# Kernel optimization log

Hardware: AMD Instinct MI355X
Metric: run time of the kernel (lower is better)

Reference implementation:

```python
import jax, jax.numpy as jnp
import numpy as np

HIDDEN = 160
LN_EPS = 1e-5


def _gru_dir(x_seq, Wih, Whh, bih, bhh, reverse):
    # x_seq: [B,T,D] -> hidden states [B,T,H] (PyTorch GRU gate math)
    B = x_seq.shape[0]
    xW = jnp.einsum('btd,gd->btg', x_seq, Wih) + bih  # [B,T,3H]
    if reverse:
        xW = xW[:, ::-1]

    def step(h, xw):
        g = h @ Whh.T + bhh
        xr, xz, xn = jnp.split(xw, 3, axis=-1)
        hr, hz, hn = jnp.split(g, 3, axis=-1)
        r = jax.nn.sigmoid(xr + hr)
        z = jax.nn.sigmoid(xz + hz)
        n = jnp.tanh(xn + r * hn)
        h_new = (1.0 - z) * n + z * h
        return h_new, h_new

    h0 = jnp.zeros((B, HIDDEN), dtype=x_seq.dtype)
    _, hs = jax.lax.scan(step, h0, jnp.swapaxes(xW, 0, 1))  # [T,B,H]
    hs = jnp.swapaxes(hs, 0, 1)  # [B,T,H]
    if reverse:
        hs = hs[:, ::-1]
    return hs


def _bigru_layer(x_seq, Wih, Whh, bih, bhh):
    f = _gru_dir(x_seq, Wih[0], Whh[0], bih[0], bhh[0], False)
    b = _gru_dir(x_seq, Wih[1], Whh[1], bih[1], bhh[1], True)
    return jnp.concatenate([f, b], axis=-1)  # [B,T,2H]


def setup_inputs() -> dict:
    key = jax.random.key(0)
    ks = jax.random.split(key, 16)
    s = 0.1  # keep activations in a sane range
    d = {
        'x': jax.random.normal(ks[0], (64, 512, 128), jnp.float32),
        'Wih0': s * jax.random.normal(ks[1], (2, 480, 128), jnp.float32),
        'Whh0': s * jax.random.normal(ks[2], (2, 480, 160), jnp.float32),
        'bih0': s * jax.random.normal(ks[3], (2, 480), jnp.float32),
        'bhh0': s * jax.random.normal(ks[4], (2, 480), jnp.float32),
        'Wih1': s * jax.random.normal(ks[5], (2, 480, 320), jnp.float32),
        'Whh1': s * jax.random.normal(ks[6], (2, 480, 160), jnp.float32),
        'bih1': s * jax.random.normal(ks[7], (2, 480), jnp.float32),
        'bhh1': s * jax.random.normal(ks[8], (2, 480), jnp.float32),
        'key_w': s * jax.random.normal(ks[9], (160, 320), jnp.float32),
        'key_b': s * jax.random.normal(ks[10], (160,), jnp.float32),
        'score_w': s * jax.random.normal(ks[11], (4, 160), jnp.float32),
        'score_b': s * jax.random.normal(ks[12], (4,), jnp.float32),
        'proj_w': s * jax.random.normal(ks[13], (256, 320), jnp.float32),
        'proj_b': s * jax.random.normal(ks[14], (256,), jnp.float32),
        'ln_g': jnp.ones((256,), jnp.float32),
        'ln_b': jnp.zeros((256,), jnp.float32),
    }
    return d


def reference(x, Wih0, Whh0, bih0, bhh0, Wih1, Whh1, bih1, bhh1,
              key_w, key_b, score_w, score_b, proj_w, proj_b, ln_g, ln_b):
    # bi-GRU, 2 layers (dropout off in eval)
    h1 = _bigru_layer(x, Wih0, Whh0, bih0, bhh0)   # [B,T,2H]
    seq_out = _bigru_layer(h1, Wih1, Whh1, bih1, bhh1)  # [B,T,2H]

    keys = jnp.tanh(seq_out @ key_w.T + key_b)           # [B,T,H]
    attn_logits = keys @ score_w.T + score_b             # [B,T,heads]

    # motion bias: per-frame displacement norm, z-normalized over time (std is unbiased)
    motion = jnp.linalg.norm(x[:, 1:] - x[:, :-1], axis=-1, keepdims=True)  # [B,T-1,1]
    motion = jnp.concatenate([motion[:, :1], motion], axis=1)               # [B,T,1]
    motion = (motion - motion.mean(axis=1, keepdims=True)) / (
        motion.std(axis=1, keepdims=True, ddof=1) + 1e-6)

    weights = jax.nn.softmax(attn_logits + motion, axis=1)  # [B,T,heads]

    # sum over time of per-head weighted seq_out, then mean over heads
    n_heads = weights.shape[-1]
    pooled = jnp.einsum('btd,bth->bd', seq_out, weights) / n_heads  # [B,2H]

    embedding = pooled @ proj_w.T + proj_b  # dropout=identity in eval
    mu = embedding.mean(axis=-1, keepdims=True)
    var = embedding.var(axis=-1, keepdims=True)
    embedding = (embedding - mu) * jax.lax.rsqrt(var + LN_EPS) * ln_g + ln_b
    embedding = embedding / jnp.maximum(
        jnp.linalg.norm(embedding, axis=-1, keepdims=True), 1e-12)

    return embedding, weights.mean(axis=2)
```

## Files before the change

kernel.cpp:

```cpp
#include <hip/hip_runtime.h>
#include <hip/hip_bf16.h>
#include <math.h>

#define T_SEQ 512
#define BATCH 64
#define DIN   128
#define H     160
#define G3    480

typedef _Float16 half8_t __attribute__((ext_vector_type(8)));
typedef _Float16 half4_t __attribute__((ext_vector_type(4)));
typedef _Float16 half2_t __attribute__((ext_vector_type(2)));
typedef float    f32x4   __attribute__((ext_vector_type(4)));

__device__ __forceinline__ float sigmoidf_(float x) {
    return 1.0f / (1.0f + __expf(-x));
}
__device__ __forceinline__ float tanhf_(float x) {
    float a = fabsf(x);
    float e = __expf(2.0f * a);
    float t = 1.0f - 2.0f / (e + 1.0f);
    return copysignf(t, x);
}

__device__ __forceinline__ void dot8(const half8_t h, const half8_t w,
                                     float& a0, float& a1, float& a2, float& a3) {
#if __has_builtin(__builtin_amdgcn_fdot2)
    half2_t h01{h[0], h[1]}, h23{h[2], h[3]}, h45{h[4], h[5]}, h67{h[6], h[7]};
    half2_t w01{w[0], w[1]}, w23{w[2], w[3]}, w45{w[4], w[5]}, w67{w[6], w[7]};
    a0 = __builtin_amdgcn_fdot2(h01, w01, a0, false);
    a1 = __builtin_amdgcn_fdot2(h23, w23, a1, false);
    a2 = __builtin_amdgcn_fdot2(h45, w45, a2, false);
    a3 = __builtin_amdgcn_fdot2(h67, w67, a3, false);
#else
    a0 += (float)h[0] * (float)w[0] + (float)h[1] * (float)w[1];
    a1 += (float)h[2] * (float)w[2] + (float)h[3] * (float)w[3];
    a2 += (float)h[4] * (float)w[4] + (float)h[5] * (float)w[5];
    a3 += (float)h[6] * (float)w[6] + (float)h[7] * (float)w[7];
#endif
}

__device__ __forceinline__ float blockReduceSum(float v, float* red) {
    #pragma unroll
    for (int off = 32; off > 0; off >>= 1) v += __shfl_down(v, off, 64);
    int wave = threadIdx.x >> 6, lane = threadIdx.x & 63;
    __syncthreads();
    if (lane == 0) red[wave] = v;
    __syncthreads();
    float s = red[0];
    int nw = blockDim.x >> 6;
    for (int i = 1; i < nw; ++i) s += red[i];
    return s;
}
__device__ __forceinline__ float blockReduceMax(float v, float* red) {
    #pragma unroll
    for (int off = 32; off > 0; off >>= 1) v = fmaxf(v, __shfl_down(v, off, 64));
    int wave = threadIdx.x >> 6, lane = threadIdx.x & 63;
    __syncthreads();
    if (lane == 0) red[wave] = v;
    __syncthreads();
    float s = red[0];
    int nw = blockDim.x >> 6;
    for (int i = 1; i < nw; ++i) s = fmaxf(s, red[i]);
    return s;
}

__global__ __launch_bounds__(256) void cvt_f2h_kernel(
    const float* __restrict__ src, _Float16* __restrict__ dst, int n4)
{
    int i = blockIdx.x * 256 + threadIdx.x;
    int stride = gridDim.x * 256;
    for (; i < n4; i += stride) {
        float4 v = reinterpret_cast<const float4*>(src)[i];
        half4_t h = {(_Float16)v.x, (_Float16)v.y, (_Float16)v.z, (_Float16)v.w};
        reinterpret_cast<half4_t*>(dst)[i] = h;
    }
}

template<int LDSK>
__global__ __launch_bounds__(256) void gemm_f16_mfma_kernel(
    const _Float16* __restrict__ A, const _Float16* __restrict__ B,
    const float* __restrict__ bias, float* __restrict__ C,
    int N, int K, int act)
{
    __shared__ _Float16 Bs[64][LDSK];
    int tid  = threadIdx.x;
    int lane = tid & 63, wave = tid >> 6;
    int row0 = blockIdx.x * 64, col0 = blockIdx.y * 64;
    int kc8 = K >> 3;
    for (int idx = tid; idx < 64 * kc8; idx += 256) {
        int rr = idx / kc8, kc = (idx - rr * kc8) << 3;
        int gcol = col0 + rr;
        half8_t v = {};
        if (gcol < N) v = *reinterpret_cast<const half8_t*>(B + (size_t)gcol * K + kc);
        *reinterpret_cast<half8_t*>(&Bs[rr][kc]) = v;
    }
    __syncthreads();

    f32x4 acc0 = {}, acc1 = {}, acc2 = {}, acc3 = {};
    int arow = row0 + wave * 16 + (lane & 15);
    int koff = (lane >> 4) << 3;
    const _Float16* ap = A + (size_t)arow * K + koff;
    int bl = lane & 15;
    for (int k0 = 0; k0 < K; k0 += 32) {
        half8_t a8 = *reinterpret_cast<const half8_t*>(ap + k0);
        half8_t b0 = *reinterpret_cast<const half8_t*>(&Bs[bl     ][k0 + koff]);
        half8_t b1 = *reinterpret_cast<const half8_t*>(&Bs[bl + 16][k0 + koff]);
        half8_t b2 = *reinterpret_cast<const half8_t*>(&Bs[bl + 32][k0 + koff]);
        half8_t b3 = *reinterpret_cast<const half8_t*>(&Bs[bl + 48][k0 + koff]);
        acc0 = __builtin_amdgcn_mfma_f32_16x16x32_f16(a8, b0, acc0, 0, 0, 0);
        acc1 = __builtin_amdgcn_mfma_f32_16x16x32_f16(a8, b1, acc1, 0, 0, 0);
        acc2 = __builtin_amdgcn_mfma_f32_16x16x32_f16(a8, b2, acc2, 0, 0, 0);
        acc3 = __builtin_amdgcn_mfma_f32_16x16x32_f16(a8, b3, acc3, 0, 0, 0);
    }

    int crow = row0 + wave * 16 + ((lane >> 4) << 2);
    int cb   = col0 + (lane & 15);
    f32x4 accs[4] = {acc0, acc1, acc2, acc3};
    #pragma unroll
    for (int j = 0; j < 4; ++j) {
        int ccol = cb + j * 16;
        if (ccol < N) {
            float bv = bias[ccol];
            #pragma unroll
            for (int i = 0; i < 4; ++i) {
                float v = accs[j][i] + bv;
                if (act) v = tanhf_(v);
                C[(size_t)(crow + i) * N + ccol] = v;
            }
        }
    }
}

__global__ __launch_bounds__(512)
__attribute__((amdgpu_waves_per_eu(2, 2)))
void gru_kernel(
    const float* __restrict__ xw, const _Float16* __restrict__ whh_h,
    const float* __restrict__ bhh, _Float16* __restrict__ out)
{
    int b    = blockIdx.x >> 1;
    int dir  = blockIdx.x & 1;
    int tid  = threadIdx.x;
    bool active = (tid < G3);
    int rc   = active ? tid : 0;
    __shared__ __align__(16) _Float16 h_h[H];
    __shared__ float g_s[G3];

    const _Float16* wp = whh_h + (size_t)dir * G3 * H + (size_t)rc * H;
    float4 f0, f1, f2, f3, f4, f5, f6, f7, f8, f9;
    float4 f10, f11, f12, f13, f14, f15, f16, f17, f18, f19;
    asm volatile("global_load_dwordx4 %0, %1, off"            : "=&v"(f0)  : "v"(wp));
    asm volatile("global_load_dwordx4 %0, %1, off offset:16"  : "=&v"(f1)  : "v"(wp));
    asm volatile("global_load_dwordx4 %0, %1, off offset:32"  : "=&v"(f2)  : "v"(wp));
    asm volatile("global_load_dwordx4 %0, %1, off offset:48"  : "=&v"(f3)  : "v"(wp));
    asm volatile("global_load_dwordx4 %0, %1, off offset:64"  : "=&v"(f4)  : "v"(wp));
    asm volatile("global_load_dwordx4 %0, %1, off offset:80"  : "=&v"(f5)  : "v"(wp));
    asm volatile("global_load_dwordx4 %0, %1, off offset:96"  : "=&v"(f6)  : "v"(wp));
    asm volatile("global_load_dwordx4 %0, %1, off offset:112" : "=&v"(f7)  : "v"(wp));
    asm volatile("global_load_dwordx4 %0, %1, off offset:128" : "=&v"(f8)  : "v"(wp));
    asm volatile("global_load_dwordx4 %0, %1, off offset:144" : "=&v"(f9)  : "v"(wp));
    asm volatile("global_load_dwordx4 %0, %1, off offset:160" : "=&v"(f10) : "v"(wp));
    asm volatile("global_load_dwordx4 %0, %1, off offset:176" : "=&v"(f11) : "v"(wp));
    asm volatile("global_load_dwordx4 %0, %1, off offset:192" : "=&v"(f12) : "v"(wp));
    asm volatile("global_load_dwordx4 %0, %1, off offset:208" : "=&v"(f13) : "v"(wp));
    asm volatile("global_load_dwordx4 %0, %1, off offset:224" : "=&v"(f14) : "v"(wp));
    asm volatile("global_load_dwordx4 %0, %1, off offset:240" : "=&v"(f15) : "v"(wp));
    asm volatile("global_load_dwordx4 %0, %1, off offset:256" : "=&v"(f16) : "v"(wp));
    asm volatile("global_load_dwordx4 %0, %1, off offset:272" : "=&v"(f17) : "v"(wp));
    asm volatile("global_load_dwordx4 %0, %1, off offset:288" : "=&v"(f18) : "v"(wp));
    asm volatile("global_load_dwordx4 %0, %1, off offset:304" : "=&v"(f19) : "v"(wp));
    float bias = bhh[dir * G3 + rc];
    asm volatile("s_waitcnt vmcnt(0)" ::: "memory");
    __builtin_amdgcn_sched_barrier(0);
    half8_t w0  = __builtin_bit_cast(half8_t, f0);
    half8_t w1  = __builtin_bit_cast(half8_t, f1);
    half8_t w2  = __builtin_bit_cast(half8_t, f2);
    half8_t w3  = __builtin_bit_cast(half8_t, f3);
    half8_t w4  = __builtin_bit_cast(half8_t, f4);
    half8_t w5  = __builtin_bit_cast(half8_t, f5);
    half8_t w6  = __builtin_bit_cast(half8_t, f6);
    half8_t w7  = __builtin_bit_cast(half8_t, f7);
    half8_t w8  = __builtin_bit_cast(half8_t, f8);
    half8_t w9  = __builtin_bit_cast(half8_t, f9);
    half8_t w10 = __builtin_bit_cast(half8_t, f10);
    half8_t w11 = __builtin_bit_cast(half8_t, f11);
    half8_t w12 = __builtin_bit_cast(half8_t, f12);
    half8_t w13 = __builtin_bit_cast(half8_t, f13);
    half8_t w14 = __builtin_bit_cast(half8_t, f14);
    half8_t w15 = __builtin_bit_cast(half8_t, f15);
    half8_t w16 = __builtin_bit_cast(half8_t, f16);
    half8_t w17 = __builtin_bit_cast(half8_t, f17);
    half8_t w18 = __builtin_bit_cast(half8_t, f18);
    half8_t w19 = __builtin_bit_cast(half8_t, f19);

    if (tid < H) h_h[tid] = (_Float16)0.f;
    float hcur = 0.f;
    __syncthreads();

    float xr = 0.f, xz = 0.f, xn = 0.f;
    {
        int tt0 = dir ? (T_SEQ - 1) : 0;
        size_t base0 = ((size_t)b * T_SEQ + tt0) * 960 + (size_t)dir * G3;
        if (tid < H) {
            xr = xw[base0 + tid];
            xz = xw[base0 + H + tid];
            xn = xw[base0 + 2 * H + tid];
        }
    }

    for (int step = 0; step < T_SEQ; ++step) {
        int tt = dir ? (T_SEQ - 1 - step) : step;
        float nxr = 0.f, nxz = 0.f, nxn = 0.f;
        {
            int sn  = (step + 1 < T_SEQ) ? step + 1 : step;
            int ttn = dir ? (T_SEQ - 1 - sn) : sn;
            size_t basen = ((size_t)b * T_SEQ + ttn) * 960 + (size_t)dir * G3;
            if (tid < H) {
                nxr = xw[basen + tid];
                nxz = xw[basen + H + tid];
                nxn = xw[basen + 2 * H + tid];
            }
        }
        float a0 = 0.f, a1 = 0.f, a2 = 0.f, a3 = 0.f;
        {
            const half8_t* hp8 = reinterpret_cast<const half8_t*>(h_h);
            dot8(hp8[0],  w0,  a0, a1, a2, a3);
            dot8(hp8[1],  w1,  a0, a1, a2, a3);
            dot8(hp8[2],  w2,  a0, a1, a2, a3);
            dot8(hp8[3],  w3,  a0, a1, a2, a3);
            dot8(hp8[4],  w4,  a0, a1, a2, a3);
            dot8(hp8[5],  w5,  a0, a1, a2, a3);
            dot8(hp8[6],  w6,  a0, a1, a2, a3);
            dot8(hp8[7],  w7,  a0, a1, a2, a3);
            dot8(hp8[8],  w8,  a0, a1, a2, a3);
            dot8(hp8[9],  w9,  a0, a1, a2, a3);
            dot8(hp8[10], w10, a0, a1, a2, a3);
            dot8(hp8[11], w11, a0, a1, a2, a3);
            dot8(hp8[12], w12, a0, a1, a2, a3);
            dot8(hp8[13], w13, a0, a1, a2, a3);
            dot8(hp8[14], w14, a0, a1, a2, a3);
            dot8(hp8[15], w15, a0, a1, a2, a3);
            dot8(hp8[16], w16, a0, a1, a2, a3);
            dot8(hp8[17], w17, a0, a1, a2, a3);
            dot8(hp8[18], w18, a0, a1, a2, a3);
            dot8(hp8[19], w19, a0, a1, a2, a3);
        }
        if (active) g_s[tid] = (a0 + a1) + (a2 + a3) + bias;
        __syncthreads();
        if (tid < H) {
            float rg = sigmoidf_(xr + g_s[tid]);
            float z  = sigmoidf_(xz + g_s[H + tid]);
            float n  = tanhf_(xn + rg * g_s[2 * H + tid]);
            float hn = (1.0f - z) * n + z * hcur;
            hcur = hn;
            h_h[tid] = (_Float16)hn;
            out[((size_t)b * T_SEQ + tt) * 320 + (size_t)dir * H + tid] = (_Float16)hn;
        }
        __syncthreads();
        xr = nxr; xz = nxz; xn = nxn;
    }
}

__global__ __launch_bounds__(256) void logits_kernel(
    const float* __restrict__ keys, const float* __restrict__ sw,
    const float* __restrict__ sb, float* __restrict__ out)
{
    int gid = blockIdx.x * 256 + threadIdx.x;
    int tok = gid >> 2, h = gid & 3;
    const float4* kr = reinterpret_cast<const float4*>(keys + (size_t)tok * H);
    const float4* wr = reinterpret_cast<const float4*>(sw + (size_t)h * H);
    float acc = 0.f;
    #pragma unroll
    for (int i = 0; i < H / 4; ++i) {
        float4 a = kr[i], w4 = wr[i];
        acc += a.x * w4.x + a.y * w4.y + a.z * w4.z + a.w * w4.w;
    }
    out[gid] = acc + sb[h];
}

__global__ __launch_bounds__(512) void final_kernel(
    const float* __restrict__ x, const float* __restrict__ logits,
    const _Float16* __restrict__ seq, const float* __restrict__ proj_w,
    const float* __restrict__ proj_b, const float* __restrict__ ln_g,
    const float* __restrict__ ln_b, float* __restrict__ out)
{
    int b   = blockIdx.x;
    int tid = threadIdx.x;
    __shared__ float ms[T_SEQ];
    __shared__ float ss[T_SEQ];
    __shared__ __align__(16) float pooled[320];
    __shared__ float red[8];

    {
        float m = 0.f;
        if (tid >= 1) {
            const float4* xc = reinterpret_cast<const float4*>(x + ((size_t)b * T_SEQ + tid) * DIN);
            const float4* xp = reinterpret_cast<const float4*>(x + ((size_t)b * T_SEQ + tid - 1) * DIN);
            float s = 0.f;
            #pragma unroll
            for (int i = 0; i < DIN / 4; ++i) {
                float4 a = xc[i], p = xp[i];
                float dx = a.x - p.x, dy = a.y - p.y, dz = a.z - p.z, dw = a.w - p.w;
                s += dx * dx + dy * dy + dz * dz + dw * dw;
            }
            m = sqrtf(s);
        }
        ms[tid] = m;
    }
    __syncthreads();
    if (tid == 0) ms[0] = ms[1];
    __syncthreads();
    float mv   = ms[tid];
    float mean = blockReduceSum(mv, red) * (1.0f / T_SEQ);
    float var  = blockReduceSum((mv - mean) * (mv - mean), red) * (1.0f / (T_SEQ - 1));
    float mstd = (mv - mean) / (sqrtf(var) + 1e-6f);

    float4 lg = *reinterpret_cast<const float4*>(logits + ((size_t)b * T_SEQ + tid) * 4);
    float l[4] = {lg.x + mstd, lg.y + mstd, lg.z + mstd, lg.w + mstd};
    float ssum = 0.f;
    #pragma unroll
    for (int h = 0; h < 4; ++h) {
        float mx = blockReduceMax(l[h], red);
        float e  = __expf(l[h] - mx);
        float se = blockReduceSum(e, red);
        float wv = e / se;
        ssum += wv;
    }
    float sv = ssum * 0.25f;
    ss[tid] = sv;
    out[16384 + b * T_SEQ + tid] = sv;
    __syncthreads();

    if (tid < 320) {
        float acc = 0.f;
        const _Float16* sp = seq + (size_t)b * T_SEQ * 320 + tid;
        #pragma unroll 4
        for (int t = 0; t < T_SEQ; ++t) acc += (float)sp[(size_t)t * 320] * ss[t];
        pooled[tid] = acc;
    }
    __syncthreads();

    float e = 0.f;
    if (tid < 256) {
        const float4* pw = reinterpret_cast<const float4*>(proj_w + (size_t)tid * 320);
        const float4* pl = reinterpret_cast<const float4*>(pooled);
        float acc = 0.f;
        #pragma unroll
        for (int i = 0; i < 80; ++i) {
            float4 w4 = pw[i], p4 = pl[i];
            acc += w4.x * p4.x + w4.y * p4.y + w4.z * p4.z + w4.w * p4.w;
        }
        e = acc + proj_b[tid];
    }
    float mu = blockReduceSum(tid < 256 ? e : 0.f, red) * (1.0f / 256);
    float dv = (tid < 256) ? (e - mu) : 0.f;
    float vr = blockReduceSum(dv * dv, red) * (1.0f / 256);
    float g  = 0.f;
    if (tid < 256) g = (e - mu) * rsqrtf(vr + 1e-5f) * ln_g[tid] + ln_b[tid];
    float nrm = sqrtf(blockReduceSum(g * g, red));
    nrm = fmaxf(nrm, 1e-12f);
    if (tid < 256) out[b * 256 + tid] = g / nrm;
}

extern "C" void kernel_launch(void* const* d_in, const int* in_sizes, int n_in,
                              void* d_out, int out_size, void* d_ws, size_t ws_size,
                              hipStream_t stream) {
    const float* x       = (const float*)d_in[0];
    const float* Wih0    = (const float*)d_in[1];
    const float* Whh0    = (const float*)d_in[2];
    const float* bih0    = (const float*)d_in[3];
    const float* bhh0    = (const float*)d_in[4];
    const float* Wih1    = (const float*)d_in[5];
    const float* Whh1    = (const float*)d_in[6];
    const float* bih1    = (const float*)d_in[7];
    const float* bhh1    = (const float*)d_in[8];
    const float* key_w   = (const float*)d_in[9];
    const float* key_b   = (const float*)d_in[10];
    const float* score_w = (const float*)d_in[11];
    const float* score_b = (const float*)d_in[12];
    const float* proj_w  = (const float*)d_in[13];
    const float* proj_b  = (const float*)d_in[14];
    const float* ln_g    = (const float*)d_in[15];
    const float* ln_b    = (const float*)d_in[16];

    const int M  = BATCH * T_SEQ;
    const int NW = 2 * G3 * H;

    float* ws    = (float*)d_ws;
    float* xwbuf = ws;
    float* keys  = xwbuf + 31457280;
    float* lgts  = keys + 5242880;
    _Float16* h1_h   = (_Float16*)(lgts + 131072);
    _Float16* seq_h  = h1_h + 10485760;
    _Float16* x_h    = seq_h + 10485760;
    _Float16* whh_h  = x_h + 4194304;
    _Float16* wih0_h = whh_h + 2 * NW;
    _Float16* wih1_h = wih0_h + 122880;
    _Float16* keyw_h = wih1_h + 307200;
    float* outf  = (float*)d_out;

    cvt_f2h_kernel<<<150, 256, 0, stream>>>(Whh0, whh_h, NW / 4);
    cvt_f2h_kernel<<<150, 256, 0, stream>>>(Whh1, whh_h + NW, NW / 4);
    cvt_f2h_kernel<<<120, 256, 0, stream>>>(Wih0, wih0_h, 122880 / 4);
    cvt_f2h_kernel<<<300, 256, 0, stream>>>(Wih1, wih1_h, 307200 / 4);
    cvt_f2h_kernel<<<50,  256, 0, stream>>>(key_w, keyw_h, 51200 / 4);
    cvt_f2h_kernel<<<2048, 256, 0, stream>>>(x, x_h, 4194304 / 4);

    gemm_f16_mfma_kernel<144><<<dim3(M / 64, 15), 256, 0, stream>>>(
        x_h, wih0_h, bih0, xwbuf, 960, 128, 0);
    gru_kernel<<<128, 512, 0, stream>>>(xwbuf, whh_h, bhh0, h1_h);
    gemm_f16_mfma_kernel<336><<<dim3(M / 64, 15), 256, 0, stream>>>(
        h1_h, wih1_h, bih1, xwbuf, 960, 320, 0);
    gru_kernel<<<128, 512, 0, stream>>>(xwbuf, whh_h + NW, bhh1, seq_h);
    gemm_f16_mfma_kernel<336><<<dim3(M / 64, 3), 256, 0, stream>>>(
        seq_h, keyw_h, key_b, keys, 160, 320, 1);
    logits_kernel<<<512, 256, 0, stream>>>(keys, score_w, score_b, lgts);
    final_kernel<<<64, 512, 0, stream>>>(x, lgts, seq_h, proj_w, proj_b, ln_g, ln_b, outf);
}
```

Baseline: 1.206 ms.

## Merge GRU forward and backward directions into one 1024-thread block

Each GRU block now handles both directions of one batch element, with 512 threads per direction, instead of one block per (batch, direction). Per-direction hidden state and gate buffers are indexed in shared memory. The weight loads use plain vector loads in place of the hand-written asm with an explicit waitcnt, and the waves_per_eu hint is removed. This halves the block count and enlarges each barrier, and the 1024-thread launch bound tightens the register budget for the register-resident weights.

```diff
diff --git a/kernel.cpp b/kernel.cpp
--- a/kernel.cpp
+++ b/kernel.cpp
@@ -132,68 +132,30 @@
     }
 }
 
-__global__ __launch_bounds__(512)
-__attribute__((amdgpu_waves_per_eu(2, 2)))
-void gru_kernel(
+__global__ __launch_bounds__(1024) void gru_kernel(
     const float* __restrict__ xw, const _Float16* __restrict__ whh_h,
     const float* __restrict__ bhh, _Float16* __restrict__ out)
 {
-    int b    = blockIdx.x >> 1;
-    int dir  = blockIdx.x & 1;
+    int b    = blockIdx.x;
     int tid  = threadIdx.x;
-    bool active = (tid < G3);
-    int rc   = active ? tid : 0;
-    __shared__ __align__(16) _Float16 h_h[H];
-    __shared__ float g_s[G3];
-
-    const _Float16* wp = whh_h + (size_t)dir * G3 * H + (size_t)rc * H;
-    float4 f0, f1, f2, f3, f4, f5, f6, f7, f8, f9;
-    float4 f10, f11, f12, f13, f14, f15, f16, f17, f18, f19;
-    asm volatile("global_load_dwordx4 %0, %1, off"            : "=&v"(f0)  : "v"(wp));
-    asm volatile("global_load_dwordx4 %0, %1, off offset:16"  : "=&v"(f1)  : "v"(wp));
-    asm volatile("global_load_dwordx4 %0, %1, off offset:32"  : "=&v"(f2)  : "v"(wp));
-    asm volatile("global_load_dwordx4 %0, %1, off offset:48"  : "=&v"(f3)  : "v"(wp));
-    asm volatile("global_load_dwordx4 %0, %1, off offset:64"  : "=&v"(f4)  : "v"(wp));
-    asm volatile("global_load_dwordx4 %0, %1, off offset:80"  : "=&v"(f5)  : "v"(wp));
-    asm volatile("global_load_dwordx4 %0, %1, off offset:96"  : "=&v"(f6)  : "v"(wp));
-    asm volatile("global_load_dwordx4 %0, %1, off offset:112" : "=&v"(f7)  : "v"(wp));
-    asm volatile("global_load_dwordx4 %0, %1, off offset:128" : "=&v"(f8)  : "v"(wp));
-    asm volatile("global_load_dwordx4 %0, %1, off offset:144" : "=&v"(f9)  : "v"(wp));
-    asm volatile("global_load_dwordx4 %0, %1, off offset:160" : "=&v"(f10) : "v"(wp));
-    asm volatile("global_load_dwordx4 %0, %1, off offset:176" : "=&v"(f11) : "v"(wp));
-    asm volatile("global_load_dwordx4 %0, %1, off offset:192" : "=&v"(f12) : "v"(wp));
-    asm volatile("global_load_dwordx4 %0, %1, off offset:208" : "=&v"(f13) : "v"(wp));
-    asm volatile("global_load_dwordx4 %0, %1, off offset:224" : "=&v"(f14) : "v"(wp));
-    asm volatile("global_load_dwordx4 %0, %1, off offset:240" : "=&v"(f15) : "v"(wp));
-    asm volatile("global_load_dwordx4 %0, %1, off offset:256" : "=&v"(f16) : "v"(wp));
-    asm volatile("global_load_dwordx4 %0, %1, off offset:272" : "=&v"(f17) : "v"(wp));
-    asm volatile("global_load_dwordx4 %0, %1, off offset:288" : "=&v"(f18) : "v"(wp));
-    asm volatile("global_load_dwordx4 %0, %1, off offset:304" : "=&v"(f19) : "v"(wp));
+    int dir  = tid >> 9;
+    int l    = tid & 511;
+    bool rowact = (l < G3);
+    int rc   = rowact ? l : 0;
+    bool gact = (l < H);
+    __shared__ __align__(16) _Float16 h_h[2][H];
+    __shared__ float g_s[2][G3];
+
+    const half8_t* wp8 = reinterpret_cast<const half8_t*>(
+        whh_h + ((size_t)dir * G3 + rc) * H);
+    half8_t w0  = wp8[0],  w1  = wp8[1],  w2  = wp8[2],  w3  = wp8[3];
+    half8_t w4  = wp8[4],  w5  = wp8[5],  w6  = wp8[6],  w7  = wp8[7];
+    half8_t w8  = wp8[8],  w9  = wp8[9],  w10 = wp8[10], w11 = wp8[11];
+    half8_t w12 = wp8[12], w13 = wp8[13], w14 = wp8[14], w15 = wp8[15];
+    half8_t w16 = wp8[16], w17 = wp8[17], w18 = wp8[18], w19 = wp8[19];
     float bias = bhh[dir * G3 + rc];
-    asm volatile("s_waitcnt vmcnt(0)" ::: "memory");
-    __builtin_amdgcn_sched_barrier(0);
-    half8_t w0  = __builtin_bit_cast(half8_t, f0);
-    half8_t w1  = __builtin_bit_cast(half8_t, f1);
-    half8_t w2  = __builtin_bit_cast(half8_t, f2);
-    half8_t w3  = __builtin_bit_cast(half8_t, f3);
-    half8_t w4  = __builtin_bit_cast(half8_t, f4);
-    half8_t w5  = __builtin_bit_cast(half8_t, f5);
-    half8_t w6  = __builtin_bit_cast(half8_t, f6);
-    half8_t w7  = __builtin_bit_cast(half8_t, f7);
-    half8_t w8  = __builtin_bit_cast(half8_t, f8);
-    half8_t w9  = __builtin_bit_cast(half8_t, f9);
-    half8_t w10 = __builtin_bit_cast(half8_t, f10);
-    half8_t w11 = __builtin_bit_cast(half8_t, f11);
-    half8_t w12 = __builtin_bit_cast(half8_t, f12);
-    half8_t w13 = __builtin_bit_cast(half8_t, f13);
-    half8_t w14 = __builtin_bit_cast(half8_t, f14);
-    half8_t w15 = __builtin_bit_cast(half8_t, f15);
-    half8_t w16 = __builtin_bit_cast(half8_t, f16);
-    half8_t w17 = __builtin_bit_cast(half8_t, f17);
-    half8_t w18 = __builtin_bit_cast(half8_t, f18);
-    half8_t w19 = __builtin_bit_cast(half8_t, f19);
-
-    if (tid < H) h_h[tid] = (_Float16)0.f;
+
+    if (gact) h_h[dir][l] = (_Float16)0.f;
     float hcur = 0.f;
     __syncthreads();
 
@@ -201,10 +163,10 @@
     {
         int tt0 = dir ? (T_SEQ - 1) : 0;
         size_t base0 = ((size_t)b * T_SEQ + tt0) * 960 + (size_t)dir * G3;
-        if (tid < H) {
-            xr = xw[base0 + tid];
-            xz = xw[base0 + H + tid];
-            xn = xw[base0 + 2 * H + tid];
+        if (gact) {
+            xr = xw[base0 + l];
+            xz = xw[base0 + H + l];
+            xn = xw[base0 + 2 * H + l];
         }
     }
 
@@ -215,15 +177,15 @@
             int sn  = (step + 1 < T_SEQ) ? step + 1 : step;
             int ttn = dir ? (T_SEQ - 1 - sn) : sn;
             size_t basen = ((size_t)b * T_SEQ + ttn) * 960 + (size_t)dir * G3;
-            if (tid < H) {
-                nxr = xw[basen + tid];
-                nxz = xw[basen + H + tid];
-                nxn = xw[basen + 2 * H + tid];
+            if (gact) {
+                nxr = xw[basen + l];
+                nxz = xw[basen + H + l];
+                nxn = xw[basen + 2 * H + l];
             }
         }
         float a0 = 0.f, a1 = 0.f, a2 = 0.f, a3 = 0.f;
         {
-            const half8_t* hp8 = reinterpret_cast<const half8_t*>(h_h);
+            const half8_t* hp8 = reinterpret_cast<const half8_t*>(&h_h[dir][0]);
             dot8(hp8[0],  w0,  a0, a1, a2, a3);
             dot8(hp8[1],  w1,  a0, a1, a2, a3);
             dot8(hp8[2],  w2,  a0, a1, a2, a3);
@@ -245,16 +207,16 @@
             dot8(hp8[18], w18, a0, a1, a2, a3);
             dot8(hp8[19], w19, a0, a1, a2, a3);
         }
-        if (active) g_s[tid] = (a0 + a1) + (a2 + a3) + bias;
+        if (rowact) g_s[dir][l] = (a0 + a1) + (a2 + a3) + bias;
         __syncthreads();
-        if (tid < H) {
-            float rg = sigmoidf_(xr + g_s[tid]);
-            float z  = sigmoidf_(xz + g_s[H + tid]);
-            float n  = tanhf_(xn + rg * g_s[2 * H + tid]);
+        if (gact) {
+            float rg = sigmoidf_(xr + g_s[dir][l]);
+            float z  = sigmoidf_(xz + g_s[dir][H + l]);
+            float n  = tanhf_(xn + rg * g_s[dir][2 * H + l]);
             float hn = (1.0f - z) * n + z * hcur;
             hcur = hn;
-            h_h[tid] = (_Float16)hn;
-            out[((size_t)b * T_SEQ + tt) * 320 + (size_t)dir * H + tid] = (_Float16)hn;
+            h_h[dir][l] = (_Float16)hn;
+            out[((size_t)b * T_SEQ + tt) * 320 + (size_t)dir * H + l] = (_Float16)hn;
         }
         __syncthreads();
         xr = nxr; xz = nxz; xn = nxn;
@@ -408,10 +370,10 @@
 
     gemm_f16_mfma_kernel<144><<<dim3(M / 64, 15), 256, 0, stream>>>(
         x_h, wih0_h, bih0, xwbuf, 960, 128, 0);
-    gru_kernel<<<128, 512, 0, stream>>>(xwbuf, whh_h, bhh0, h1_h);
+    gru_kernel<<<64, 1024, 0, stream>>>(xwbuf, whh_h, bhh0, h1_h);
     gemm_f16_mfma_kernel<336><<<dim3(M / 64, 15), 256, 0, stream>>>(
         h1_h, wih1_h, bih1, xwbuf, 960, 320, 0);
-    gru_kernel<<<128, 512, 0, stream>>>(xwbuf, whh_h + NW, bhh1, seq_h);
+    gru_kernel<<<64, 1024, 0, stream>>>(xwbuf, whh_h + NW, bhh1, seq_h);
     gemm_f16_mfma_kernel<336><<<dim3(M / 64, 3), 256, 0, stream>>>(
         seq_h, keyw_h, key_b, keys, 160, 320, 1);
     logits_kernel<<<512, 256, 0, stream>>>(keys, score_w, score_b, lgts);
```

New measurement: 2.078 ms. 72.3% more time.
